# Performance work log

Hardware: AMD Instinct MI355X
Metric: run time of the kernel (lower is better)

Reference implementation:

```python
import jax, jax.numpy as jnp
import numpy as np

NP_, NA_ = 50000, 20000
D_IN, D_HID, D_OUT = 128, 128, 64
E_W, E_C, E_R = 250000, 500000, 250000


def setup_inputs() -> dict:
    key = jax.random.key(0)
    ks = jax.random.split(key, 14)
    s_in = 1.0 / np.sqrt(D_IN)
    s_h = 1.0 / np.sqrt(D_HID)
    return {
        "x_paper": jax.random.normal(ks[0], (NP_, D_IN), jnp.float32),
        "x_author": jax.random.normal(ks[1], (NA_, D_IN), jnp.float32),
        "Wl1": jax.random.normal(ks[2], (3, D_HID, D_IN), jnp.float32) * s_in,
        "bl1": jax.random.normal(ks[3], (3, D_HID), jnp.float32) * 0.01,
        "Wr1": jax.random.normal(ks[4], (3, D_HID, D_IN), jnp.float32) * s_in,
        "Wl2": jax.random.normal(ks[5], (3, D_OUT, D_HID), jnp.float32) * s_h,
        "bl2": jax.random.normal(ks[6], (3, D_OUT), jnp.float32) * 0.01,
        "Wr2": jax.random.normal(ks[7], (3, D_OUT, D_HID), jnp.float32) * s_h,
        "writes_src": jax.random.randint(ks[8], (E_W,), 0, NA_),
        "writes_dst": jax.random.randint(ks[9], (E_W,), 0, NP_),
        "cites_src": jax.random.randint(ks[10], (E_C,), 0, NP_),
        "cites_dst": jax.random.randint(ks[11], (E_C,), 0, NP_),
        "rev_src": jax.random.randint(ks[12], (E_R,), 0, NP_),
        "rev_dst": jax.random.randint(ks[13], (E_R,), 0, NA_),
    }


def _sage(x_src, x_dst, src, dst, Wl, bl, Wr, n_dst):
    # PyG SAGEConv(aggr='mean'): lin_l(mean_j x_src[j]) + lin_r(x_dst)
    agg = jax.ops.segment_sum(x_src[src], dst, num_segments=n_dst)
    cnt = jax.ops.segment_sum(jnp.ones_like(dst, dtype=x_src.dtype), dst,
                              num_segments=n_dst)
    agg = agg / jnp.maximum(cnt, 1.0)[:, None]  # degree-0 nodes -> 0 (PyG scatter-mean)
    return agg @ Wl.T + bl + x_dst @ Wr.T


def reference(x_paper, x_author, Wl1, bl1, Wr1, Wl2, bl2, Wr2,
              writes_src, writes_dst, cites_src, cites_dst, rev_src, rev_dst):
    def hetero_layer(xp, xa, Wl, bl, Wr):
        # HeteroConv(aggr='mean'): average per-relation outputs per dst node type
        op = 0.5 * (_sage(xa, xp, writes_src, writes_dst, Wl[0], bl[0], Wr[0], NP_)
                    + _sage(xp, xp, cites_src, cites_dst, Wl[1], bl[1], Wr[1], NP_))
        oa = _sage(xp, xa, rev_src, rev_dst, Wl[2], bl[2], Wr[2], NA_)
        return op, oa

    hp, ha = hetero_layer(x_paper, x_author, Wl1, bl1, Wr1)
    hp, ha = jax.nn.relu(hp), jax.nn.relu(ha)  # norm_type='none', dropout eval-mode
    hp, _ = hetero_layer(hp, ha, Wl2, bl2, Wr2)
    return hp  # logits for category='paper', [NP_, D_OUT]
```

## Files before the change

### kernel.cpp

```cpp
#include <hip/hip_runtime.h>

#define NP 50000
#define NA 20000
#define E_W 250000
#define E_C 500000
#define E_R 250000
#define E_TOT (E_W + E_C + E_R)
#define CAP 48
#define RBLK 8192
#define NSEG 123
#define NCHP 782
#define NCHA 313
#define NBIN (NCHP + NCHA)

typedef __attribute__((ext_vector_type(8))) short short8;
typedef __attribute__((ext_vector_type(4))) float floatx4;
typedef __attribute__((ext_vector_type(2))) float floatx2;

__device__ __forceinline__ unsigned short f2bf(float f) {
    unsigned u = __float_as_uint(f);
    return (unsigned short)((u + 0x7FFFu + ((u >> 16) & 1u)) >> 16);
}
__device__ __forceinline__ float bflo(unsigned v) { return __uint_as_float(v << 16); }
__device__ __forceinline__ float bfhi(unsigned v) { return __uint_as_float(v & 0xFFFF0000u); }

__device__ __forceinline__ int frag_off(int NT, int j, int n, int k) {
    int t = n >> 4, ln = n & 15;
    int kb = k >> 5, q = (k >> 3) & 3, r = k & 7;
    return (((j * NT + t) * 4 + kb) * 64 + q * 16 + ln) * 8 + r;
}

__device__ __forceinline__ void prep_body(
    int idx,
    const float* __restrict__ xp, const float* __restrict__ xa,
    const float* __restrict__ Wl1, const float* __restrict__ Wr1,
    const float* __restrict__ Wl2, const float* __restrict__ Wr2,
    const float* __restrict__ bl1, const float* __restrict__ bl2,
    unsigned short* __restrict__ xpb, unsigned short* __restrict__ xab,
    unsigned* __restrict__ xp8, unsigned* __restrict__ xa8,
    unsigned short* __restrict__ Wp1, unsigned short* __restrict__ Wa1,
    unsigned short* __restrict__ Wt2, unsigned short* __restrict__ Wr2s,
    float* __restrict__ bias_p1, float* __restrict__ bias_a1,
    float* __restrict__ bias_p2) {
    const int n4p = NP * 32, n4a = NA * 32;
    if (idx < n4p + n4a) {
        const float* s; unsigned short* d; unsigned* d8; int i = idx;
        if (i < n4p) { s = xp; d = xpb; d8 = xp8; }
        else { s = xa; d = xab; d8 = xa8; i -= n4p; }
        float4 v = ((const float4*)s)[i];
        ushort4 u;
        u.x = f2bf(v.x); u.y = f2bf(v.y); u.z = f2bf(v.z); u.w = f2bf(v.w);
        ((ushort4*)d)[i] = u;
        int w = __builtin_amdgcn_cvt_pk_fp8_f32(v.x, v.y, 0, false);
        w = __builtin_amdgcn_cvt_pk_fp8_f32(v.z, v.w, w, true);
        d8[i] = (unsigned)w;
        return;
    }
    int j = idx - (n4p + n4a);
    if (j < 49152) {
        int jj = j >> 14, rem = j & 16383, n = rem >> 7, k = rem & 127;
        float v = (jj == 0)   ? 0.5f * Wl1[rem]
                  : (jj == 1) ? 0.5f * Wl1[16384 + rem]
                              : 0.5f * (Wr1[rem] + Wr1[16384 + rem]);
        Wp1[frag_off(8, jj, n, k)] = f2bf(v);
    } else if (j < 81920) {
        int i2 = j - 49152;
        int jj = i2 >> 14, rem = i2 & 16383, n = rem >> 7, k = rem & 127;
        float v = (jj == 0) ? Wl1[2 * 16384 + rem] : Wr1[2 * 16384 + rem];
        Wa1[frag_off(8, jj, n, k)] = f2bf(v);
    } else if (j < 98304) {
        int i2 = j - 81920;
        int jj = i2 >> 13, rem = i2 & 8191, n = rem >> 7, k = rem & 127;
        float v = 0.5f * Wl2[jj * 8192 + rem];
        Wt2[frag_off(4, jj, n, k)] = f2bf(v);
    } else if (j < 106496) {
        int i2 = j - 98304;
        int n = i2 >> 7, k = i2 & 127;
        float v = 0.5f * (Wr2[i2] + Wr2[8192 + i2]);
        Wr2s[frag_off(4, 0, n, k)] = f2bf(v);
    } else if (j < 106496 + 320) {
        int b = j - 106496;
        if (b < 128) bias_p1[b] = 0.5f * (bl1[b] + bl1[128 + b]);
        else if (b < 256) bias_a1[b - 128] = bl1[256 + b - 128];
        else bias_p2[b - 256] = 0.5f * (bl2[b - 256] + bl2[64 + b - 256]);
    }
}

__device__ __forceinline__ void edge_bin(
    int e, const int* __restrict__ w_src, const int* __restrict__ w_dst,
    const int* __restrict__ c_src, const int* __restrict__ c_dst,
    const int* __restrict__ r_src, const int* __restrict__ r_dst,
    int& bin, int& sub, int& src) {
    bool isC = (e >= E_W) & (e < E_W + E_C);
    bool isR = e >= E_W + E_C;
    const int* db = isR ? r_dst : (isC ? c_dst : w_dst);
    const int* sb = isR ? r_src : (isC ? c_src : w_src);
    int idx = e - (isC ? E_W : 0) - (isR ? (E_W + E_C) : 0);
    int d = db[idx];
    src = sb[idx];
    if (isR) { bin = NCHP + (d >> 6); sub = d & 63; }
    else { bin = d >> 6; sub = (d & 63) + (isC ? 64 : 0); }
}

__device__ __forceinline__ void route_body(
    int bid, const int* __restrict__ w_src, const int* __restrict__ w_dst,
    const int* __restrict__ c_src, const int* __restrict__ c_dst,
    const int* __restrict__ r_src, const int* __restrict__ r_dst,
    unsigned* __restrict__ seg, unsigned* __restrict__ segmeta,
    int* cnt_s, int* base_s, int* cur_s) {
    int tid = threadIdx.x, lane = tid & 63;
    for (int k = tid; k < NBIN; k += 512) cnt_s[k] = 0;
    __syncthreads();
#pragma unroll 4
    for (int u = 0; u < 16; ++u) {
        int e = bid * RBLK + u * 512 + tid;
        if (e < E_TOT) {
            int bin, sub, src;
            edge_bin(e, w_src, w_dst, c_src, c_dst, r_src, r_dst, bin, sub, src);
            atomicAdd(&cnt_s[bin], 1);
        }
    }
    __syncthreads();
    if (tid < 64) {
        int v[18], tot = 0;
#pragma unroll
        for (int q = 0; q < 18; ++q) {
            int k = tid * 18 + q;
            v[q] = (k < NBIN) ? cnt_s[k] : 0;
            tot += v[q];
        }
        int sc = tot;
#pragma unroll
        for (int ofs = 1; ofs < 64; ofs <<= 1) {
            int t = __shfl_up(sc, ofs, 64);
            if (lane >= ofs) sc += t;
        }
        int run = sc - tot;
#pragma unroll
        for (int q = 0; q < 18; ++q) {
            int k = tid * 18 + q;
            if (k < NBIN) { base_s[k] = run; run += v[q]; }
        }
    }
    __syncthreads();
    for (int k = tid; k < NBIN; k += 512) {
        segmeta[bid * NBIN + k] = ((unsigned)base_s[k] << 16) | (unsigned)cnt_s[k];
        cur_s[k] = base_s[k];
    }
    __syncthreads();
    unsigned* segb = seg + (size_t)bid * RBLK;
#pragma unroll 4
    for (int u = 0; u < 16; ++u) {
        int e = bid * RBLK + u * 512 + tid;
        if (e < E_TOT) {
            int bin, sub, src;
            edge_bin(e, w_src, w_dst, c_src, c_dst, r_src, r_dst, bin, sub, src);
            int pos = atomicAdd(&cur_s[bin], 1);
            segb[pos] = (unsigned)src | ((unsigned)sub << 16);
        }
    }
}

__global__ __launch_bounds__(512) void route_prep(
    const float* xp, const float* xa, const float* Wl1, const float* Wr1,
    const float* Wl2, const float* Wr2, const float* bl1, const float* bl2,
    unsigned short* xpb, unsigned short* xab, unsigned* xp8, unsigned* xa8,
    unsigned short* Wp1, unsigned short* Wa1, unsigned short* Wt2, unsigned short* Wr2s,
    float* bias_p1, float* bias_a1, float* bias_p2,
    const int* w_src, const int* w_dst, const int* c_src, const int* c_dst,
    const int* r_src, const int* r_dst,
    unsigned* seg, unsigned* segmeta) {
    __shared__ int cnt_s[NBIN], base_s[NBIN], cur_s[NBIN];
    if ((int)blockIdx.x < NSEG)
        route_body(blockIdx.x, w_src, w_dst, c_src, c_dst, r_src, r_dst,
                   seg, segmeta, cnt_s, base_s, cur_s);
    else
        prep_body((blockIdx.x - NSEG) * 512 + threadIdx.x, xp, xa, Wl1, Wr1, Wl2, Wr2,
                  bl1, bl2, xpb, xab, xp8, xa8, Wp1, Wa1, Wt2, Wr2s,
                  bias_p1, bias_a1, bias_p2);
}

__global__ __launch_bounds__(512) void fill_l1(
    const unsigned* __restrict__ seg, const unsigned* __restrict__ segmeta,
    int* __restrict__ cnt, unsigned short* __restrict__ csr,
    const unsigned* __restrict__ xp8, const unsigned* __restrict__ xa8,
    const unsigned short* __restrict__ xpb, const unsigned short* __restrict__ xab,
    const unsigned short* __restrict__ Wp1, const float* __restrict__ bias_p1,
    const unsigned short* __restrict__ Wa1, const float* __restrict__ bias_a1,
    const unsigned short* __restrict__ Wt2, const unsigned short* __restrict__ Wr2s,
    unsigned short* __restrict__ ta, unsigned short* __restrict__ tp,
    float* __restrict__ sp) {
    __shared__ unsigned short rows[128 * CAP];
    __shared__ int cursor[128];
    __shared__ unsigned pkd[NSEG];
    __shared__ __align__(16) unsigned short aggL[128][136];
    int tid = threadIdx.x;
    int k = blockIdx.x;
    bool isPaper = k < NCHP;
    int base = isPaper ? k * 64 : (k - NCHP) * 64;
    int total = isPaper ? NP : NA;
    int M = total - base; if (M > 64) M = 64;

    for (int s = tid; s < NSEG; s += 512) pkd[s] = segmeta[s * NBIN + k];
    if (tid < 128) cursor[tid] = 0;
    __syncthreads();
    {
        int grp = tid >> 4, gl = tid & 15;
        for (int s = grp; s < NSEG; s += 32) {
            unsigned pk = pkd[s];
            int n = pk & 0xFFFFu;
            const unsigned* spq = seg + (size_t)s * RBLK + (pk >> 16);
            for (int i = gl; i < n; i += 16) {
                unsigned v = spq[i];
                int sub = v >> 16, srcn = v & 0xFFFFu;
                int pos = atomicAdd(&cursor[sub], 1);
                if (pos < CAP) rows[sub * CAP + pos] = (unsigned short)srcn;
            }
        }
    }
    __syncthreads();
    {
        const unsigned* s0 = isPaper ? xa8 : xp8;
        const unsigned* s1 = xp8;
        int d0 = isPaper ? NA : NP, d1 = NP;
        int LROWS = isPaper ? 128 : 64;
        int g = tid >> 5, sl = tid & 31;
        for (int l0 = g; l0 < LROWS; l0 += 32) {
            int lA = l0, lB = l0 + 16;
            const unsigned* sA = (lA & 64) ? s1 : s0;
            const unsigned* sB = (lB & 64) ? s1 : s0;
            int duA = (lA & 64) ? d1 : d0;
            int duB = (lB & 64) ? d1 : d0;
            int dA = cursor[lA], dB = cursor[lB];
            int cA = dA < CAP ? dA : CAP, cB = dB < CAP ? dB : CAP;
            int cm = cA > cB ? cA : cB;
            const unsigned short* rpA = &rows[lA * CAP];
            const unsigned short* rpB = &rows[lB * CAP];
            float a0 = 0.f, a1 = 0.f, a2 = 0.f, a3 = 0.f;
            float b0 = 0.f, b1 = 0.f, b2 = 0.f, b3 = 0.f;
            for (int i = 0; i < cm; i += 8) {
                short8 rA = *(const short8*)&rpA[i];
                short8 rB = *(const short8*)&rpB[i];
                unsigned vA[8], vB[8];
#pragma unroll
                for (int u = 0; u < 8; ++u) {
                    int q = (i + u < cA) ? (int)(unsigned short)rA[u] : duA;
                    vA[u] = sA[(q << 5) + sl];
                }
#pragma unroll
                for (int u = 0; u < 8; ++u) {
                    int q = (i + u < cB) ? (int)(unsigned short)rB[u] : duB;
                    vB[u] = sB[(q << 5) + sl];
                }
#pragma unroll
                for (int u = 0; u < 8; ++u) {
                    floatx2 lo = __builtin_amdgcn_cvt_pk_f32_fp8(vA[u], false);
                    floatx2 hi = __builtin_amdgcn_cvt_pk_f32_fp8(vA[u], true);
                    a0 += lo.x; a1 += lo.y; a2 += hi.x; a3 += hi.y;
                }
#pragma unroll
                for (int u = 0; u < 8; ++u) {
                    floatx2 lo = __builtin_amdgcn_cvt_pk_f32_fp8(vB[u], false);
                    floatx2 hi = __builtin_amdgcn_cvt_pk_f32_fp8(vB[u], true);
                    b0 += lo.x; b1 += lo.y; b2 += hi.x; b3 += hi.y;
                }
            }
            float sclA = dA > 0 ? 1.f / (float)dA : 0.f;
            float sclB = dB > 0 ? 1.f / (float)dB : 0.f;
            unsigned wloA = ((unsigned)f2bf(a1 * sclA) << 16) | (unsigned)f2bf(a0 * sclA);
            unsigned whiA = ((unsigned)f2bf(a3 * sclA) << 16) | (unsigned)f2bf(a2 * sclA);
            unsigned wloB = ((unsigned)f2bf(b1 * sclB) << 16) | (unsigned)f2bf(b0 * sclB);
            unsigned whiB = ((unsigned)f2bf(b3 * sclB) << 16) | (unsigned)f2bf(b2 * sclB);
            *(uint2*)&aggL[lA][sl * 4] = make_uint2(wloA, whiA);
            *(uint2*)&aggL[lB][sl * 4] = make_uint2(wloB, whiB);
        }
    }
    __syncthreads();
    int wave = tid >> 6, lane = tid & 63, ln = lane & 15, quad = lane >> 4;
    int wrow = (wave & 3) * 16, nhalf = wave >> 2;
    floatx4 acc[4];
#pragma unroll
    for (int t = 0; t < 4; ++t) acc[t] = (floatx4){0.f, 0.f, 0.f, 0.f};
    auto gemm_lds = [&](const unsigned short* __restrict__ Wb, int rowoff) {
#pragma unroll
        for (int kb = 0; kb < 4; ++kb) {
            short8 af = *(const short8*)&aggL[rowoff + wrow + ln][quad * 8 + kb * 32];
#pragma unroll
            for (int t = 0; t < 4; ++t) {
                short8 bf = *(const short8*)(Wb + ((nhalf * 4 + t) * 4 + kb) * 512 + lane * 8);
                acc[t] = __builtin_amdgcn_mfma_f32_16x16x32_bf16(af, bf, acc[t], 0, 0, 0);
            }
        }
    };
    auto gemm_glob = [&](const unsigned short* __restrict__ X,
                         const unsigned short* __restrict__ Wb) {
        int row = base + wrow + ln;
        int rowc = row < total ? row : total - 1;
        const unsigned short* A = X + (size_t)rowc * 128 + quad * 8;
#pragma unroll
        for (int kb = 0; kb < 4; ++kb) {
            short8 af = *(const short8*)(A + kb * 32);
#pragma unroll
            for (int t = 0; t < 4; ++t) {
                short8 bf = *(const short8*)(Wb + ((nhalf * 4 + t) * 4 + kb) * 512 + lane * 8);
                acc[t] = __builtin_amdgcn_mfma_f32_16x16x32_bf16(af, bf, acc[t], 0, 0, 0);
            }
        }
    };
    if (isPaper) {
        gemm_lds(Wp1, 0);
        gemm_lds(Wp1 + 16384, 64);
        gemm_glob(xpb, Wp1 + 2 * 16384);
    } else {
        gemm_lds(Wa1, 0);
        gemm_glob(xab, Wa1 + 16384);
    }
    __syncthreads();
    {
        const float* bias = isPaper ? bias_p1 : bias_a1;
#pragma unroll
        for (int t = 0; t < 4; ++t) {
            int col = nhalf * 64 + t * 16 + ln;
            float bv = bias[col];
#pragma unroll
            for (int r = 0; r < 4; ++r)
                aggL[wrow + quad * 4 + r][col] = f2bf(fmaxf(acc[t][r] + bv, 0.f));
        }
    }
    __syncthreads();
    floatx4 tacc[4];
#pragma unroll
    for (int t = 0; t < 4; ++t) tacc[t] = (floatx4){0.f, 0.f, 0.f, 0.f};
    int rows16 = (wave & 3) * 16;
    if (isPaper) {
        const unsigned short* W = (wave < 4) ? (Wt2 + 64 * 128) : Wr2s;
#pragma unroll
        for (int kb = 0; kb < 4; ++kb) {
            short8 af = *(const short8*)&aggL[rows16 + ln][quad * 8 + kb * 32];
#pragma unroll
            for (int t = 0; t < 4; ++t) {
                short8 bf = *(const short8*)(W + (t * 4 + kb) * 512 + lane * 8);
                tacc[t] = __builtin_amdgcn_mfma_f32_16x16x32_bf16(af, bf, tacc[t], 0, 0, 0);
            }
        }
#pragma unroll
        for (int t = 0; t < 4; ++t) {
            int col = t * 16 + ln;
#pragma unroll
            for (int r = 0; r < 4; ++r) {
                int lr = rows16 + quad * 4 + r;
                if (lr < M) {
                    if (wave < 4) tp[(size_t)(base + lr) * 64 + col] = f2bf(tacc[t][r]);
                    else sp[(size_t)(base + lr) * 64 + col] = tacc[t][r];
                }
            }
        }
    } else {
        int thalf = wave >> 2;
#pragma unroll
        for (int kb = 0; kb < 4; ++kb) {
            short8 af = *(const short8*)&aggL[rows16 + ln][quad * 8 + kb * 32];
#pragma unroll
            for (int tt = 0; tt < 2; ++tt) {
                short8 bf = *(const short8*)(Wt2 + ((thalf * 2 + tt) * 4 + kb) * 512 + lane * 8);
                tacc[tt] = __builtin_amdgcn_mfma_f32_16x16x32_bf16(af, bf, tacc[tt], 0, 0, 0);
            }
        }
#pragma unroll
        for (int tt = 0; tt < 2; ++tt) {
            int col = (thalf * 2 + tt) * 16 + ln;
#pragma unroll
            for (int r = 0; r < 4; ++r) {
                int lr = rows16 + quad * 4 + r;
                if (lr < M) ta[(size_t)(base + lr) * 64 + col] = f2bf(tacc[tt][r]);
            }
        }
    }
    if (isPaper) {
        for (int r = tid; r < 2 * M; r += 512)
            cnt[base * 2 + r] = cursor[(r >> 1) + ((r & 1) << 6)];
        const unsigned* rU = (const unsigned*)rows;
        unsigned* cU = (unsigned*)csr + (size_t)base * 2 * (CAP / 2);
        for (int i = tid; i < 2 * M * (CAP / 2); i += 512) {
            int r = i / (CAP / 2), j = i - r * (CAP / 2);
            cU[i] = rU[((r >> 1) + ((r & 1) << 6)) * (CAP / 2) + j];
        }
    }
}

__global__ void agg2(const unsigned short* __restrict__ ta, const unsigned short* __restrict__ tp,
                     const int* __restrict__ cnt, const unsigned short* __restrict__ csr,
                     const float* __restrict__ sp_in, const float* __restrict__ bias_p2,
                     float* __restrict__ out) {
    int node = blockIdx.x * 8 + (threadIdx.x >> 5);
    if (node >= NP) return;
    int lane = threadIdx.x & 63;
    int sl = lane & 31;
    int hw = lane & 32;
    const unsigned* t0p = (const unsigned*)ta;
    const unsigned* t1p = (const unsigned*)tp;
    int deg0 = cnt[node * 2], deg1 = cnt[node * 2 + 1];
    int c0 = deg0 < CAP ? deg0 : CAP;
    int c1 = deg1 < CAP ? deg1 : CAP;
    const unsigned short* row0 = csr + (size_t)node * 2 * CAP;
    const unsigned short* row1 = row0 + CAP;
    int e00 = (sl < c0) ? (int)row0[sl] : NA;
    int e01 = (32 + sl < c0) ? (int)row0[32 + sl] : NA;
    int e10 = (sl < c1) ? (int)row1[sl] : NP;
    int e11 = (32 + sl < c1) ? (int)row1[32 + sl] : NP;
    int degw = c0 > c1 ? c0 : c1;
    int other = __shfl_xor(degw, 32, 64);
    if (other > degw) degw = other;
    float sa0 = 0.f, sa1 = 0.f, sb0 = 0.f, sb1 = 0.f;
    float ua0 = 0.f, ua1 = 0.f, ub0 = 0.f, ub1 = 0.f;
    for (int i = 0; i < degw; i += 8) {
        unsigned v0[8], v1[8];
#pragma unroll
        for (int u = 0; u < 8; ++u) {
            int ii = i + u;
            int es = (ii < 32) ? e00 : e01;
            int qq = __shfl(es, hw | (ii & 31), 64);
            qq = (ii < c0) ? qq : NA;
            v0[u] = t0p[(qq << 5) + sl];
        }
#pragma unroll
        for (int u = 0; u < 8; ++u) {
            int ii = i + u;
            int es = (ii < 32) ? e10 : e11;
            int qq = __shfl(es, hw | (ii & 31), 64);
            qq = (ii < c1) ? qq : NP;
            v1[u] = t1p[(qq << 5) + sl];
        }
#pragma unroll
        for (int u = 0; u < 8; ++u) {
            if (u & 1) { sb0 += bflo(v0[u]); sb1 += bfhi(v0[u]); }
            else       { sa0 += bflo(v0[u]); sa1 += bfhi(v0[u]); }
        }
#pragma unroll
        for (int u = 0; u < 8; ++u) {
            if (u & 1) { ub0 += bflo(v1[u]); ub1 += bfhi(v1[u]); }
            else       { ua0 += bflo(v1[u]); ua1 += bfhi(v1[u]); }
        }
    }
    float scl0 = deg0 > 0 ? 1.f / (float)deg0 : 0.f;
    float scl1 = deg1 > 0 ? 1.f / (float)deg1 : 0.f;
    float r0 = (sa0 + sb0) * scl0 + (ua0 + ub0) * scl1;
    float r1 = (sa1 + sb1) * scl0 + (ua1 + ub1) * scl1;
    float2 spv = ((const float2*)sp_in)[(size_t)node * 32 + sl];
    float2 bv = ((const float2*)bias_p2)[sl];
    ((float2*)out)[(size_t)node * 32 + sl] =
        make_float2(r0 + spv.x + bv.x, r1 + spv.y + bv.y);
}

extern "C" void kernel_launch(void* const* d_in, const int* in_sizes, int n_in,
                              void* d_out, int out_size, void* d_ws, size_t ws_size,
                              hipStream_t stream) {
    (void)in_sizes; (void)n_in; (void)out_size; (void)ws_size;
    const float* xp  = (const float*)d_in[0];
    const float* xa  = (const float*)d_in[1];
    const float* Wl1 = (const float*)d_in[2];
    const float* bl1 = (const float*)d_in[3];
    const float* Wr1 = (const float*)d_in[4];
    const float* Wl2 = (const float*)d_in[5];
    const float* bl2 = (const float*)d_in[6];
    const float* Wr2 = (const float*)d_in[7];
    const int* w_src = (const int*)d_in[8];
    const int* w_dst = (const int*)d_in[9];
    const int* c_src = (const int*)d_in[10];
    const int* c_dst = (const int*)d_in[11];
    const int* r_src = (const int*)d_in[12];
    const int* r_dst = (const int*)d_in[13];
    float* out = (float*)d_out;

    char* p = (char*)d_ws;
    auto alloc = [&](size_t bytes) {
        char* r = p;
        p += (bytes + 255) & ~(size_t)255;
        return r;
    };
    unsigned short* xpb   = (unsigned short*)alloc((size_t)NP * 128 * 2);
    unsigned short* xab   = (unsigned short*)alloc((size_t)NA * 128 * 2);
    unsigned*       xp8   = (unsigned*)alloc((size_t)(NP + 1) * 128);
    unsigned*       xa8   = (unsigned*)alloc((size_t)(NA + 1) * 128);
    unsigned short* ta    = (unsigned short*)alloc((size_t)(NA + 1) * 64 * 2);
    unsigned short* tp    = (unsigned short*)alloc((size_t)(NP + 1) * 64 * 2);
    float*          sp    = (float*)alloc((size_t)NP * 64 * 4);
    int*            cnt     = (int*)alloc((size_t)NP * 2 * 4);
    unsigned short* csr     = (unsigned short*)alloc((size_t)NP * 2 * CAP * 2);
    unsigned*       seg     = (unsigned*)alloc((size_t)NSEG * RBLK * 4);
    unsigned*       segmeta = (unsigned*)alloc((size_t)NSEG * NBIN * 4);
    unsigned short* Wp1  = (unsigned short*)alloc(3 * 128 * 128 * 2);
    unsigned short* Wa1  = (unsigned short*)alloc(2 * 128 * 128 * 2);
    unsigned short* Wt2  = (unsigned short*)alloc(2 * 64 * 128 * 2);
    unsigned short* Wr2s = (unsigned short*)alloc(64 * 128 * 2);
    float* bias_p1 = (float*)alloc(128 * 4);
    float* bias_a1 = (float*)alloc(128 * 4);
    float* bias_p2 = (float*)alloc(64 * 4);

    hipMemsetAsync(xp8 + (size_t)NP * 32, 0, 128, stream);
    hipMemsetAsync(xa8 + (size_t)NA * 32, 0, 128, stream);
    hipMemsetAsync(ta + (size_t)NA * 64, 0, 128, stream);
    hipMemsetAsync(tp + (size_t)NP * 64, 0, 128, stream);

    int prep_threads = (NP + NA) * 32 + 106496 + 320;
    int prep_blocks = (prep_threads + 511) / 512;
    route_prep<<<NSEG + prep_blocks, 512, 0, stream>>>(
        xp, xa, Wl1, Wr1, Wl2, Wr2, bl1, bl2,
        xpb, xab, xp8, xa8, Wp1, Wa1, Wt2, Wr2s, bias_p1, bias_a1, bias_p2,
        w_src, w_dst, c_src, c_dst, r_src, r_dst, seg, segmeta);

    fill_l1<<<NBIN, 512, 0, stream>>>(seg, segmeta, cnt, csr,
                                      xp8, xa8, xpb, xab, Wp1, bias_p1, Wa1, bias_a1,
                                      Wt2, Wr2s, ta, tp, sp);

    agg2<<<(NP + 7) / 8, 256, 0, stream>>>(ta, tp, cnt, csr, sp, bias_p2, out);
}
```

Baseline: 199.5 us.

## Fold pad memsets into prep, widen gather to 4 rows, overlap root GEMM

The four hipMemsetAsync calls that zero the padding rows are removed and done by extra threads in the prep kernel, which cuts launch overhead. The fp8 neighbor gather in fill_l1 now handles four destination rows per thread group instead of two, so more loads are in flight. The root-feature GEMM that reads from global memory is moved ahead of the barrier so it overlaps the LDS aggregation. The costs are higher register pressure from the 4x8 load buffer, and the GEMM now runs before aggL is guaranteed complete, which relies on it not reading aggL.

After: 198.3 us. Within noise of the previous version (-0.6%).

```diff
diff --git a/kernel.cpp b/kernel.cpp
--- a/kernel.cpp
+++ b/kernel.cpp
@@ -41,7 +41,8 @@
     unsigned short* __restrict__ Wp1, unsigned short* __restrict__ Wa1,
     unsigned short* __restrict__ Wt2, unsigned short* __restrict__ Wr2s,
     float* __restrict__ bias_p1, float* __restrict__ bias_a1,
-    float* __restrict__ bias_p2) {
+    float* __restrict__ bias_p2,
+    unsigned short* __restrict__ ta, unsigned short* __restrict__ tp) {
     const int n4p = NP * 32, n4a = NA * 32;
     if (idx < n4p + n4a) {
         const float* s; unsigned short* d; unsigned* d8; int i = idx;
@@ -83,6 +84,12 @@
         if (b < 128) bias_p1[b] = 0.5f * (bl1[b] + bl1[128 + b]);
         else if (b < 256) bias_a1[b - 128] = bl1[256 + b - 128];
         else bias_p2[b - 256] = 0.5f * (bl2[b - 256] + bl2[64 + b - 256]);
+    } else if (j < 106496 + 320 + 128) {
+        int b = j - (106496 + 320);
+        if (b < 32) xp8[NP * 32 + b] = 0;
+        else if (b < 64) xa8[NA * 32 + (b - 32)] = 0;
+        else if (b < 96) ((unsigned*)ta)[NA * 32 + (b - 64)] = 0;
+        else ((unsigned*)tp)[NP * 32 + (b - 96)] = 0;
     }
 }
 
@@ -169,7 +176,8 @@
     float* bias_p1, float* bias_a1, float* bias_p2,
     const int* w_src, const int* w_dst, const int* c_src, const int* c_dst,
     const int* r_src, const int* r_dst,
-    unsigned* seg, unsigned* segmeta) {
+    unsigned* seg, unsigned* segmeta,
+    unsigned short* ta, unsigned short* tp) {
     __shared__ int cnt_s[NBIN], base_s[NBIN], cur_s[NBIN];
     if ((int)blockIdx.x < NSEG)
         route_body(blockIdx.x, w_src, w_dst, c_src, c_dst, r_src, r_dst,
@@ -177,7 +185,7 @@
     else
         prep_body((blockIdx.x - NSEG) * 512 + threadIdx.x, xp, xa, Wl1, Wr1, Wl2, Wr2,
                   bl1, bl2, xpb, xab, xp8, xa8, Wp1, Wa1, Wt2, Wr2s,
-                  bias_p1, bias_a1, bias_p2);
+                  bias_p1, bias_a1, bias_p2, ta, tp);
 }
 
 __global__ __launch_bounds__(512) void fill_l1(
@@ -225,57 +233,53 @@
         int d0 = isPaper ? NA : NP, d1 = NP;
         int LROWS = isPaper ? 128 : 64;
         int g = tid >> 5, sl = tid & 31;
-        for (int l0 = g; l0 < LROWS; l0 += 32) {
-            int lA = l0, lB = l0 + 16;
-            const unsigned* sA = (lA & 64) ? s1 : s0;
-            const unsigned* sB = (lB & 64) ? s1 : s0;
-            int duA = (lA & 64) ? d1 : d0;
-            int duB = (lB & 64) ? d1 : d0;
-            int dA = cursor[lA], dB = cursor[lB];
-            int cA = dA < CAP ? dA : CAP, cB = dB < CAP ? dB : CAP;
-            int cm = cA > cB ? cA : cB;
-            const unsigned short* rpA = &rows[lA * CAP];
-            const unsigned short* rpB = &rows[lB * CAP];
-            float a0 = 0.f, a1 = 0.f, a2 = 0.f, a3 = 0.f;
-            float b0 = 0.f, b1 = 0.f, b2 = 0.f, b3 = 0.f;
+        for (int l0 = g; l0 < LROWS; l0 += 64) {
+            const unsigned* sr = (l0 & 64) ? s1 : s0;
+            int du = (l0 & 64) ? d1 : d0;
+            int dg[4], cc[4];
+            const unsigned short* rp[4];
+            int cm = 0;
+#pragma unroll
+            for (int j = 0; j < 4; ++j) {
+                int l = l0 + j * 16;
+                dg[j] = cursor[l];
+                cc[j] = dg[j] < CAP ? dg[j] : CAP;
+                cm = cc[j] > cm ? cc[j] : cm;
+                rp[j] = &rows[l * CAP];
+            }
+            float a0[4], a1[4], a2[4], a3[4];
+#pragma unroll
+            for (int j = 0; j < 4; ++j) { a0[j] = 0.f; a1[j] = 0.f; a2[j] = 0.f; a3[j] = 0.f; }
             for (int i = 0; i < cm; i += 8) {
-                short8 rA = *(const short8*)&rpA[i];
-                short8 rB = *(const short8*)&rpB[i];
-                unsigned vA[8], vB[8];
-#pragma unroll
-                for (int u = 0; u < 8; ++u) {
-                    int q = (i + u < cA) ? (int)(unsigned short)rA[u] : duA;
-                    vA[u] = sA[(q << 5) + sl];
+                unsigned v[4][8];
+#pragma unroll
+                for (int j = 0; j < 4; ++j) {
+                    short8 rr = *(const short8*)&rp[j][i];
+#pragma unroll
+                    for (int u = 0; u < 8; ++u) {
+                        int q = (i + u < cc[j]) ? (int)(unsigned short)rr[u] : du;
+                        v[j][u] = sr[(q << 5) + sl];
+                    }
                 }
 #pragma unroll
-                for (int u = 0; u < 8; ++u) {
-                    int q = (i + u < cB) ? (int)(unsigned short)rB[u] : duB;
-                    vB[u] = sB[(q << 5) + sl];
+                for (int j = 0; j < 4; ++j) {
+#pragma unroll
+                    for (int u = 0; u < 8; ++u) {
+                        floatx2 lo = __builtin_amdgcn_cvt_pk_f32_fp8(v[j][u], false);
+                        floatx2 hi = __builtin_amdgcn_cvt_pk_f32_fp8(v[j][u], true);
+                        a0[j] += lo.x; a1[j] += lo.y; a2[j] += hi.x; a3[j] += hi.y;
+                    }
                 }
-#pragma unroll
-                for (int u = 0; u < 8; ++u) {
-                    floatx2 lo = __builtin_amdgcn_cvt_pk_f32_fp8(vA[u], false);
-                    floatx2 hi = __builtin_amdgcn_cvt_pk_f32_fp8(vA[u], true);
-                    a0 += lo.x; a1 += lo.y; a2 += hi.x; a3 += hi.y;
-                }
-#pragma unroll
-                for (int u = 0; u < 8; ++u) {
-                    floatx2 lo = __builtin_amdgcn_cvt_pk_f32_fp8(vB[u], false);
-                    floatx2 hi = __builtin_amdgcn_cvt_pk_f32_fp8(vB[u], true);
-                    b0 += lo.x; b1 += lo.y; b2 += hi.x; b3 += hi.y;
-                }
-            }
-            float sclA = dA > 0 ? 1.f / (float)dA : 0.f;
-            float sclB = dB > 0 ? 1.f / (float)dB : 0.f;
-            unsigned wloA = ((unsigned)f2bf(a1 * sclA) << 16) | (unsigned)f2bf(a0 * sclA);
-            unsigned whiA = ((unsigned)f2bf(a3 * sclA) << 16) | (unsigned)f2bf(a2 * sclA);
-            unsigned wloB = ((unsigned)f2bf(b1 * sclB) << 16) | (unsigned)f2bf(b0 * sclB);
-            unsigned whiB = ((unsigned)f2bf(b3 * sclB) << 16) | (unsigned)f2bf(b2 * sclB);
-            *(uint2*)&aggL[lA][sl * 4] = make_uint2(wloA, whiA);
-            *(uint2*)&aggL[lB][sl * 4] = make_uint2(wloB, whiB);
-        }
-    }
-    __syncthreads();
+            }
+#pragma unroll
+            for (int j = 0; j < 4; ++j) {
+                float scl = dg[j] > 0 ? 1.f / (float)dg[j] : 0.f;
+                unsigned wlo = ((unsigned)f2bf(a1[j] * scl) << 16) | (unsigned)f2bf(a0[j] * scl);
+                unsigned whi = ((unsigned)f2bf(a3[j] * scl) << 16) | (unsigned)f2bf(a2[j] * scl);
+                *(uint2*)&aggL[l0 + j * 16][sl * 4] = make_uint2(wlo, whi);
+            }
+        }
+    }
     int wave = tid >> 6, lane = tid & 63, ln = lane & 15, quad = lane >> 4;
     int wrow = (wave & 3) * 16, nhalf = wave >> 2;
     floatx4 acc[4];
@@ -307,13 +311,14 @@
             }
         }
     };
+    if (isPaper) gemm_glob(xpb, Wp1 + 2 * 16384);
+    else gemm_glob(xab, Wa1 + 16384);
+    __syncthreads();
     if (isPaper) {
         gemm_lds(Wp1, 0);
         gemm_lds(Wp1 + 16384, 64);
-        gemm_glob(xpb, Wp1 + 2 * 16384);
     } else {
         gemm_lds(Wa1, 0);
-        gemm_glob(xab, Wa1 + 16384);
     }
     __syncthreads();
     {
@@ -497,17 +502,12 @@
     float* bias_a1 = (float*)alloc(128 * 4);
     float* bias_p2 = (float*)alloc(64 * 4);
 
-    hipMemsetAsync(xp8 + (size_t)NP * 32, 0, 128, stream);
-    hipMemsetAsync(xa8 + (size_t)NA * 32, 0, 128, stream);
-    hipMemsetAsync(ta + (size_t)NA * 64, 0, 128, stream);
-    hipMemsetAsync(tp + (size_t)NP * 64, 0, 128, stream);
-
-    int prep_threads = (NP + NA) * 32 + 106496 + 320;
+    int prep_threads = (NP + NA) * 32 + 106496 + 320 + 128;
     int prep_blocks = (prep_threads + 511) / 512;
     route_prep<<<NSEG + prep_blocks, 512, 0, stream>>>(
         xp, xa, Wl1, Wr1, Wl2, Wr2, bl1, bl2,
         xpb, xab, xp8, xa8, Wp1, Wa1, Wt2, Wr2s, bias_p1, bias_a1, bias_p2,
-        w_src, w_dst, c_src, c_dst, r_src, r_dst, seg, segmeta);
+        w_src, w_dst, c_src, c_dst, r_src, r_dst, seg, segmeta, ta, tp);
 
     fill_l1<<<NBIN, 512, 0, stream>>>(seg, segmeta, cnt, csr,
                                       xp8, xa8, xpb, xab, Wp1, bias_p1, Wa1, bias_a1,
```
